# Kernel tuning notes

Hardware: AMD Instinct MI355X
Metric: run time of the kernel (lower is better)

Reference implementation:

```python
import jax, jax.numpy as jnp
import numpy as np

B, H, SQ, SKV, D = 2, 16, 2048, 3072, 64
NUM_PT = 1024  # SKV = NUM_PT + SQ


def setup_inputs() -> dict:
    key = jax.random.key(0)
    kq, kk, kv = jax.random.split(key, 3)
    q = jax.random.normal(kq, (B, H, SQ, D), dtype=jnp.float32)
    k = jax.random.normal(kk, (B, H, SKV, D), dtype=jnp.float32)
    v = jax.random.normal(kv, (B, H, SKV, D), dtype=jnp.float32)
    return {"q": q, "k": k, "v": v, "num_pt": NUM_PT}


def _prefix_causal_mask(sq, skv, num_pt):
    # kv_idx < num_pt always visible (global prefix); otherwise causal on
    # shifted index: q_idx >= kv_idx - num_pt
    q_idx = jnp.arange(sq)[:, None]   # [SQ,1]
    kv_idx = jnp.arange(skv)[None, :]  # [1,SKV]
    return (kv_idx < num_pt) | (q_idx >= kv_idx - num_pt)  # [SQ,SKV]


def reference(q, k, v, num_pt):
    scale = 1.0 / jnp.sqrt(jnp.asarray(q.shape[-1], q.dtype))
    # [B,H,SQ,SKV]
    scores = jnp.einsum("bhqd,bhkd->bhqk", q, k) * scale
    mask = _prefix_causal_mask(q.shape[2], k.shape[2], num_pt)  # [SQ,SKV]
    neg = jnp.asarray(jnp.finfo(scores.dtype).min, scores.dtype)
    scores = jnp.where(mask[None, None], scores, neg)
    probs = jax.nn.softmax(scores, axis=-1)
    return jnp.einsum("bhqk,bhkd->bhqd", probs, v)
```

## Files before the change

### kernel.cpp

```cpp
#include <hip/hip_runtime.h>

#define B_ 2
#define H_ 16
#define SQ_ 2048
#define SKV_ 3072
#define DH 64
#define QT 128
#define KVT 64
#define LDK 72

typedef __attribute__((ext_vector_type(4))) float f32x4;
typedef __attribute__((ext_vector_type(8))) short bf16x8;

__device__ __forceinline__ unsigned cvt_pk(float a, float b) {
  unsigned r;
  asm("v_cvt_pk_bf16_f32 %0, %1, %2" : "=v"(r) : "v"(a), "v"(b));
  return r;
}
__device__ __forceinline__ void pl16_swap(unsigned& a, unsigned& b) {
  asm("v_permlane16_swap_b32 %0, %1" : "+v"(a), "+v"(b));
}
__device__ __forceinline__ void pl32_swap(unsigned& a, unsigned& b) {
  asm("v_permlane32_swap_b32 %0, %1" : "+v"(a), "+v"(b));
}

#define TILE_BODY(T, RK, RV, NK, NV)                                      \
  {                                                                       \
    const int kb  = (T)*KVT;                                              \
    const int buf = (T)&1;                                                \
          \
    {                                                                     \
      int pidx = (T) + 2;                                                 \
      if (pidx > n_tiles - 1) pidx = n_tiles - 1;                         \
      const size_t nb = (size_t)pidx * KVT * DH;                          \
      NK[0] = *(const float4*)(kQp + nb);                                 \
      NK[1] = *(const float4*)(kQp + nb + 4);                             \
      NK[2] = *(const float4*)(kQp + nb + 8);                             \
      NK[3] = *(const float4*)(kQp + nb + 12);                            \
      NV[0] = *(const float4*)(vQp + nb);                                 \
      NV[1] = *(const float4*)(vQp + nb + 4);                             \
      NV[2] = *(const float4*)(vQp + nb + DH);                            \
      NV[3] = *(const float4*)(vQp + nb + DH + 4);                        \
    }                                                                     \
                   \
    f32x4 s0[4], s1[4];                                                   \
    _Pragma("unroll") for (int mg = 0; mg < 4; ++mg) {                    \
      bf16x8 ka0 = *(const bf16x8*)&Ks[buf][mg * 16 + lq][quad * 8];      \
      bf16x8 ka1 = *(const bf16x8*)&Ks[buf][mg * 16 + lq][32 + quad * 8]; \
      f32x4 c0 = (f32x4){0.f, 0.f, 0.f, 0.f};                             \
      f32x4 c1 = (f32x4){0.f, 0.f, 0.f, 0.f};                             \
      c0 = __builtin_amdgcn_mfma_f32_16x16x32_bf16(ka0, qf0[0], c0, 0, 0, 0);\
      c0 = __builtin_amdgcn_mfma_f32_16x16x32_bf16(ka1, qf0[1], c0, 0, 0, 0);\
      c1 = __builtin_amdgcn_mfma_f32_16x16x32_bf16(ka0, qf1[0], c1, 0, 0, 0);\
      c1 = __builtin_amdgcn_mfma_f32_16x16x32_bf16(ka1, qf1[1], c1, 0, 0, 0);\
      s0[mg] = c0; s1[mg] = c1;                                           \
    }                                                                     \
     \
    {                                                                     \
      union { unsigned u[4]; bf16x8 hh; } ta, tb;                         \
      ta.u[0] = cvt_pk(RK[0].x, RK[0].y);                                 \
      ta.u[1] = cvt_pk(RK[0].z, RK[0].w);                                 \
      ta.u[2] = cvt_pk(RK[1].x, RK[1].y);                                 \
      ta.u[3] = cvt_pk(RK[1].z, RK[1].w);                                 \
      *(bf16x8*)&Ks[buf ^ 1][krow][kc] = ta.hh;                           \
      tb.u[0] = cvt_pk(RK[2].x, RK[2].y);                                 \
      tb.u[1] = cvt_pk(RK[2].z, RK[2].w);                                 \
      tb.u[2] = cvt_pk(RK[3].x, RK[3].y);                                 \
      tb.u[3] = cvt_pk(RK[3].z, RK[3].w);                                 \
      *(bf16x8*)&Ks[buf ^ 1][krow][kc + 8] = tb.hh;                       \
      *(unsigned*)&Vt[buf ^ 1][vd0 + 0][2 * vp] = cvt_pk(RV[0].x, RV[2].x);\
      *(unsigned*)&Vt[buf ^ 1][vd0 + 1][2 * vp] = cvt_pk(RV[0].y, RV[2].y);\
      *(unsigned*)&Vt[buf ^ 1][vd0 + 2][2 * vp] = cvt_pk(RV[0].z, RV[2].z);\
      *(unsigned*)&Vt[buf ^ 1][vd0 + 3][2 * vp] = cvt_pk(RV[0].w, RV[2].w);\
      *(unsigned*)&Vt[buf ^ 1][vd0 + 4][2 * vp] = cvt_pk(RV[1].x, RV[3].x);\
      *(unsigned*)&Vt[buf ^ 1][vd0 + 5][2 * vp] = cvt_pk(RV[1].y, RV[3].y);\
      *(unsigned*)&Vt[buf ^ 1][vd0 + 6][2 * vp] = cvt_pk(RV[1].z, RV[3].z);\
      *(unsigned*)&Vt[buf ^ 1][vd0 + 7][2 * vp] = cvt_pk(RV[1].w, RV[3].w);\
    }                                                                     \
                   \
    if (kb + KVT - 1 > q0 + w * 32 + num_pt) {                            \
      _Pragma("unroll") for (int mg = 0; mg < 4; ++mg)                    \
        _Pragma("unroll") for (int r = 0; r < 4; ++r)                     \
          if (kb + mg * 16 + quad * 4 + r > lim0) s0[mg][r] = -__builtin_inff();\
    }                                                                     \
    if (kb + KVT - 1 > q0 + w * 32 + 16 + num_pt) {                       \
      _Pragma("unroll") for (int mg = 0; mg < 4; ++mg)                    \
        _Pragma("unroll") for (int r = 0; r < 4; ++r)                     \
          if (kb + mg * 16 + quad * 4 + r > lim1) s1[mg][r] = -__builtin_inff();\
    }                                                                     \
                                   \
    _Pragma("unroll") for (int mg = 0; mg < 4; ++mg)                      \
      _Pragma("unroll") for (int r = 0; r < 4; ++r) {                     \
        float p0 = __builtin_amdgcn_exp2f(s0[mg][r]);                     \
        float p1 = __builtin_amdgcn_exp2f(s1[mg][r]);                     \
        s0[mg][r] = p0; l40[r] += p0;                                     \
        s1[mg][r] = p1; l41[r] += p1;                                     \
      }                                                                   \
                     \
    union { unsigned u[4]; bf16x8 h; } pa00, pa01, pa10, pa11;            \
    {                                                                     \
      unsigned U[4], W[4];                                                \
      _Pragma("unroll") for (int mg = 0; mg < 4; ++mg) {                  \
        U[mg] = cvt_pk(s0[mg][0], s0[mg][1]);                             \
        W[mg] = cvt_pk(s0[mg][2], s0[mg][3]);                             \
      }                                                                   \
      pl32_swap(U[0], U[1]); pl16_swap(U[0], U[1]);                       \
      pl32_swap(W[0], W[1]); pl16_swap(W[0], W[1]);                       \
      pl32_swap(U[2], U[3]); pl16_swap(U[2], U[3]);                       \
      pl32_swap(W[2], W[3]); pl16_swap(W[2], W[3]);                       \
      pa00.u[0] = U[0]; pa00.u[1] = W[0]; pa00.u[2] = U[1]; pa00.u[3] = W[1];\
      pa01.u[0] = U[2]; pa01.u[1] = W[2]; pa01.u[2] = U[3]; pa01.u[3] = W[3];\
    }                                                                     \
    {                                                                     \
      unsigned U[4], W[4];                                                \
      _Pragma("unroll") for (int mg = 0; mg < 4; ++mg) {                  \
        U[mg] = cvt_pk(s1[mg][0], s1[mg][1]);                             \
        W[mg] = cvt_pk(s1[mg][2], s1[mg][3]);                             \
      }                                                                   \
      pl32_swap(U[0], U[1]); pl16_swap(U[0], U[1]);                       \
      pl32_swap(W[0], W[1]); pl16_swap(W[0], W[1]);                       \
      pl32_swap(U[2], U[3]); pl16_swap(U[2], U[3]);                       \
      pl32_swap(W[2], W[3]); pl16_swap(W[2], W[3]);                       \
      pa10.u[0] = U[0]; pa10.u[1] = W[0]; pa10.u[2] = U[1]; pa10.u[3] = W[1];\
      pa11.u[0] = U[2]; pa11.u[1] = W[2]; pa11.u[2] = U[3]; pa11.u[3] = W[3];\
    }                                                                     \
          \
    _Pragma("unroll") for (int dg = 0; dg < 4; ++dg) {                    \
      bf16x8 vb0 = *(const bf16x8*)&Vt[buf][dg * 16 + lq][quad * 8];      \
      bf16x8 vb1 = *(const bf16x8*)&Vt[buf][dg * 16 + lq][32 + quad * 8]; \
      O0[dg] = __builtin_amdgcn_mfma_f32_16x16x32_bf16(vb0, pa00.h, O0[dg], 0, 0, 0);\
      O0[dg] = __builtin_amdgcn_mfma_f32_16x16x32_bf16(vb1, pa01.h, O0[dg], 0, 0, 0);\
      O1[dg] = __builtin_amdgcn_mfma_f32_16x16x32_bf16(vb0, pa10.h, O1[dg], 0, 0, 0);\
      O1[dg] = __builtin_amdgcn_mfma_f32_16x16x32_bf16(vb1, pa11.h, O1[dg], 0, 0, 0);\
    }                                                                     \
    __syncthreads();                         \
  }

__global__ __launch_bounds__(256, 2) void attn_fwd(
    const float* __restrict__ qg_, const float* __restrict__ kg_,
    const float* __restrict__ vg_, const int* __restrict__ num_pt_p,
    float* __restrict__ og_) {
  __shared__ __align__(16) short Ks[2][KVT][LDK];
  __shared__ __align__(16) short Vt[2][DH][LDK];

  const int tid  = (int)threadIdx.x;
  const int lane = tid & 63;
  const int w    = tid >> 6;
  const int lq   = lane & 15;
  const int quad = lane >> 4;
  const int x    = (int)blockIdx.x;
  const int y    = (int)blockIdx.y;
  const int qb   = (y & 16) ? x : (15 - x);
  const int num_pt = *num_pt_p;
  const int q0   = qb * QT;

  const float* qg = qg_ + (size_t)y * SQ_ * DH;
  const float* kg = kg_ + (size_t)y * SKV_ * DH;
  const float* vg = vg_ + (size_t)y * SKV_ * DH;
  float*       og = og_ + (size_t)y * SQ_ * DH;

  const float SC = 0.125f * 1.44269504088896341f;

  const int qrow0 = q0 + w * 32 + lq;
  const int qrow1 = qrow0 + 16;
  bf16x8 qf0[2], qf1[2];
#pragma unroll
  for (int f = 0; f < 2; ++f) {
    const float* qp = qg + (size_t)(f ? qrow1 : qrow0) * DH + quad * 8;
#pragma unroll
    for (int kh = 0; kh < 2; ++kh) {
      float4 a = *(const float4*)(qp + kh * 32);
      float4 b = *(const float4*)(qp + kh * 32 + 4);
      union { unsigned u[4]; bf16x8 hh; } tq;
      tq.u[0] = cvt_pk(a.x * SC, a.y * SC);
      tq.u[1] = cvt_pk(a.z * SC, a.w * SC);
      tq.u[2] = cvt_pk(b.x * SC, b.y * SC);
      tq.u[3] = cvt_pk(b.z * SC, b.w * SC);
      if (f) qf1[kh] = tq.hh; else qf0[kh] = tq.hh;
    }
  }

  f32x4 O0[4], O1[4];
#pragma unroll
  for (int i = 0; i < 4; ++i) {
    O0[i] = (f32x4){0.f, 0.f, 0.f, 0.f};
    O1[i] = (f32x4){0.f, 0.f, 0.f, 0.f};
  }
  f32x4 l40 = (f32x4){0.f, 0.f, 0.f, 0.f};
  f32x4 l41 = (f32x4){0.f, 0.f, 0.f, 0.f};

  int n_tiles = (q0 + QT - 1 + num_pt) / KVT + 1;
  if (n_tiles > SKV_ / KVT) n_tiles = SKV_ / KVT;

  const int krow = tid >> 2;
  const int kc   = (tid & 3) * 16;
  const int vp   = tid & 31;
  const int vd0  = (tid >> 5) * 8;
  const float* kQp = kg + (size_t)krow * DH + kc;
  const float* vQp = vg + (size_t)(2 * vp) * DH + vd0;

  const int lim0 = qrow0 + num_pt;
  const int lim1 = qrow1 + num_pt;

  float4 Ak[4], Av[4], Bk[4], Bv[4];
  Ak[0] = *(const float4*)(kQp);
  Ak[1] = *(const float4*)(kQp + 4);
  Ak[2] = *(const float4*)(kQp + 8);
  Ak[3] = *(const float4*)(kQp + 12);
  Av[0] = *(const float4*)(vQp);
  Av[1] = *(const float4*)(vQp + 4);
  Av[2] = *(const float4*)(vQp + DH);
  Av[3] = *(const float4*)(vQp + DH + 4);
  {
    const size_t nb = (size_t)KVT * DH;
    Bk[0] = *(const float4*)(kQp + nb);
    Bk[1] = *(const float4*)(kQp + nb + 4);
    Bk[2] = *(const float4*)(kQp + nb + 8);
    Bk[3] = *(const float4*)(kQp + nb + 12);
    Bv[0] = *(const float4*)(vQp + nb);
    Bv[1] = *(const float4*)(vQp + nb + 4);
    Bv[2] = *(const float4*)(vQp + nb + DH);
    Bv[3] = *(const float4*)(vQp + nb + DH + 4);
  }
  {
    union { unsigned u[4]; bf16x8 hh; } ta, tb;
    ta.u[0] = cvt_pk(Ak[0].x, Ak[0].y);
    ta.u[1] = cvt_pk(Ak[0].z, Ak[0].w);
    ta.u[2] = cvt_pk(Ak[1].x, Ak[1].y);
    ta.u[3] = cvt_pk(Ak[1].z, Ak[1].w);
    *(bf16x8*)&Ks[0][krow][kc] = ta.hh;
    tb.u[0] = cvt_pk(Ak[2].x, Ak[2].y);
    tb.u[1] = cvt_pk(Ak[2].z, Ak[2].w);
    tb.u[2] = cvt_pk(Ak[3].x, Ak[3].y);
    tb.u[3] = cvt_pk(Ak[3].z, Ak[3].w);
    *(bf16x8*)&Ks[0][krow][kc + 8] = tb.hh;
    *(unsigned*)&Vt[0][vd0 + 0][2 * vp] = cvt_pk(Av[0].x, Av[2].x);
    *(unsigned*)&Vt[0][vd0 + 1][2 * vp] = cvt_pk(Av[0].y, Av[2].y);
    *(unsigned*)&Vt[0][vd0 + 2][2 * vp] = cvt_pk(Av[0].z, Av[2].z);
    *(unsigned*)&Vt[0][vd0 + 3][2 * vp] = cvt_pk(Av[0].w, Av[2].w);
    *(unsigned*)&Vt[0][vd0 + 4][2 * vp] = cvt_pk(Av[1].x, Av[3].x);
    *(unsigned*)&Vt[0][vd0 + 5][2 * vp] = cvt_pk(Av[1].y, Av[3].y);
    *(unsigned*)&Vt[0][vd0 + 6][2 * vp] = cvt_pk(Av[1].z, Av[3].z);
    *(unsigned*)&Vt[0][vd0 + 7][2 * vp] = cvt_pk(Av[1].w, Av[3].w);
  }
  __syncthreads();

  int t = 0;
  for (; t + 1 < n_tiles; t += 2) {
    TILE_BODY(t,     Bk, Bv, Ak, Av)
    TILE_BODY(t + 1, Ak, Av, Bk, Bv)
  }
  if (t < n_tiles) {
    TILE_BODY(t, Bk, Bv, Ak, Av)
  }

  {
    float lr = l40[0] + l40[1] + l40[2] + l40[3];
    lr += __shfl_xor(lr, 16);
    lr += __shfl_xor(lr, 32);
    float inv = 1.0f / lr;
    float* op = og + (size_t)qrow0 * DH + quad * 4;
#pragma unroll
    for (int dg = 0; dg < 4; ++dg) {
      float4 o4;
      o4.x = O0[dg][0] * inv;
      o4.y = O0[dg][1] * inv;
      o4.z = O0[dg][2] * inv;
      o4.w = O0[dg][3] * inv;
      *(float4*)(op + dg * 16) = o4;
    }
  }
  {
    float lr = l41[0] + l41[1] + l41[2] + l41[3];
    lr += __shfl_xor(lr, 16);
    lr += __shfl_xor(lr, 32);
    float inv = 1.0f / lr;
    float* op = og + (size_t)qrow1 * DH + quad * 4;
#pragma unroll
    for (int dg = 0; dg < 4; ++dg) {
      float4 o4;
      o4.x = O1[dg][0] * inv;
      o4.y = O1[dg][1] * inv;
      o4.z = O1[dg][2] * inv;
      o4.w = O1[dg][3] * inv;
      *(float4*)(op + dg * 16) = o4;
    }
  }
}

extern "C" void kernel_launch(void* const* d_in, const int* in_sizes, int n_in,
                              void* d_out, int out_size, void* d_ws, size_t ws_size,
                              hipStream_t stream) {
  const float* q = (const float*)d_in[0];
  const float* k = (const float*)d_in[1];
  const float* v = (const float*)d_in[2];
  const int* np  = (const int*)d_in[3];
  float* out = (float*)d_out;
  dim3 grid(SQ_ / QT, B_ * H_);
  attn_fwd<<<grid, dim3(256), 0, stream>>>(q, k, v, np, out);
}
```

Baseline: 156.7 us.

## Software-pipeline QK softmax of next tile with PV of current tile

Restructures the KV loop into a three-buffer LDS ring so each iteration computes QK^T and softmax for tile t+1 while doing the PV MFMAs for tile t, staging tile t+2 and prefetching tile t+3 from global. The aim is to overlap exp/convert/permlane work with matrix instructions and reduce dependency stalls. In exchange it uses more LDS (three buffers) and holds two sets of P fragments in registers, which adds register pressure and could lower occupancy at 2 blocks per CU.

Result: slower. 160.2 us (+2.2%).

```diff
diff --git a/kernel.cpp b/kernel.cpp
--- a/kernel.cpp
+++ b/kernel.cpp
@@ -12,6 +12,8 @@
 typedef __attribute__((ext_vector_type(4))) float f32x4;
 typedef __attribute__((ext_vector_type(8))) short bf16x8;
 
+struct PAset { bf16x8 p00, p01, p10, p11; };
+
 __device__ __forceinline__ unsigned cvt_pk(float a, float b) {
   unsigned r;
   asm("v_cvt_pk_bf16_f32 %0, %1, %2" : "=v"(r) : "v"(a), "v"(b));
@@ -24,29 +26,14 @@
   asm("v_permlane32_swap_b32 %0, %1" : "+v"(a), "+v"(b));
 }
 
-#define TILE_BODY(T, RK, RV, NK, NV)                                      \
-  {                                                                       \
-    const int kb  = (T)*KVT;                                              \
-    const int buf = (T)&1;                                                \
-          \
-    {                                                                     \
-      int pidx = (T) + 2;                                                 \
-      if (pidx > n_tiles - 1) pidx = n_tiles - 1;                         \
-      const size_t nb = (size_t)pidx * KVT * DH;                          \
-      NK[0] = *(const float4*)(kQp + nb);                                 \
-      NK[1] = *(const float4*)(kQp + nb + 4);                             \
-      NK[2] = *(const float4*)(kQp + nb + 8);                             \
-      NK[3] = *(const float4*)(kQp + nb + 12);                            \
-      NV[0] = *(const float4*)(vQp + nb);                                 \
-      NV[1] = *(const float4*)(vQp + nb + 4);                             \
-      NV[2] = *(const float4*)(vQp + nb + DH);                            \
-      NV[3] = *(const float4*)(vQp + nb + DH + 4);                        \
-    }                                                                     \
-                   \
+
+#define QKSM(TIDX, KSP, PAS)                                              \
+  {                                                                       \
+    const int kb = (TIDX)*KVT;                                            \
     f32x4 s0[4], s1[4];                                                   \
     _Pragma("unroll") for (int mg = 0; mg < 4; ++mg) {                    \
-      bf16x8 ka0 = *(const bf16x8*)&Ks[buf][mg * 16 + lq][quad * 8];      \
-      bf16x8 ka1 = *(const bf16x8*)&Ks[buf][mg * 16 + lq][32 + quad * 8]; \
+      bf16x8 ka0 = *(const bf16x8*)&KSP[mg * 16 + lq][quad * 8];          \
+      bf16x8 ka1 = *(const bf16x8*)&KSP[mg * 16 + lq][32 + quad * 8];     \
       f32x4 c0 = (f32x4){0.f, 0.f, 0.f, 0.f};                             \
       f32x4 c1 = (f32x4){0.f, 0.f, 0.f, 0.f};                             \
       c0 = __builtin_amdgcn_mfma_f32_16x16x32_bf16(ka0, qf0[0], c0, 0, 0, 0);\
@@ -55,29 +42,6 @@
       c1 = __builtin_amdgcn_mfma_f32_16x16x32_bf16(ka1, qf1[1], c1, 0, 0, 0);\
       s0[mg] = c0; s1[mg] = c1;                                           \
     }                                                                     \
-     \
-    {                                                                     \
-      union { unsigned u[4]; bf16x8 hh; } ta, tb;                         \
-      ta.u[0] = cvt_pk(RK[0].x, RK[0].y);                                 \
-      ta.u[1] = cvt_pk(RK[0].z, RK[0].w);                                 \
-      ta.u[2] = cvt_pk(RK[1].x, RK[1].y);                                 \
-      ta.u[3] = cvt_pk(RK[1].z, RK[1].w);                                 \
-      *(bf16x8*)&Ks[buf ^ 1][krow][kc] = ta.hh;                           \
-      tb.u[0] = cvt_pk(RK[2].x, RK[2].y);                                 \
-      tb.u[1] = cvt_pk(RK[2].z, RK[2].w);                                 \
-      tb.u[2] = cvt_pk(RK[3].x, RK[3].y);                                 \
-      tb.u[3] = cvt_pk(RK[3].z, RK[3].w);                                 \
-      *(bf16x8*)&Ks[buf ^ 1][krow][kc + 8] = tb.hh;                       \
-      *(unsigned*)&Vt[buf ^ 1][vd0 + 0][2 * vp] = cvt_pk(RV[0].x, RV[2].x);\
-      *(unsigned*)&Vt[buf ^ 1][vd0 + 1][2 * vp] = cvt_pk(RV[0].y, RV[2].y);\
-      *(unsigned*)&Vt[buf ^ 1][vd0 + 2][2 * vp] = cvt_pk(RV[0].z, RV[2].z);\
-      *(unsigned*)&Vt[buf ^ 1][vd0 + 3][2 * vp] = cvt_pk(RV[0].w, RV[2].w);\
-      *(unsigned*)&Vt[buf ^ 1][vd0 + 4][2 * vp] = cvt_pk(RV[1].x, RV[3].x);\
-      *(unsigned*)&Vt[buf ^ 1][vd0 + 5][2 * vp] = cvt_pk(RV[1].y, RV[3].y);\
-      *(unsigned*)&Vt[buf ^ 1][vd0 + 6][2 * vp] = cvt_pk(RV[1].z, RV[3].z);\
-      *(unsigned*)&Vt[buf ^ 1][vd0 + 7][2 * vp] = cvt_pk(RV[1].w, RV[3].w);\
-    }                                                                     \
-                   \
     if (kb + KVT - 1 > q0 + w * 32 + num_pt) {                            \
       _Pragma("unroll") for (int mg = 0; mg < 4; ++mg)                    \
         _Pragma("unroll") for (int r = 0; r < 4; ++r)                     \
@@ -88,7 +52,6 @@
         _Pragma("unroll") for (int r = 0; r < 4; ++r)                     \
           if (kb + mg * 16 + quad * 4 + r > lim1) s1[mg][r] = -__builtin_inff();\
     }                                                                     \
-                                   \
     _Pragma("unroll") for (int mg = 0; mg < 4; ++mg)                      \
       _Pragma("unroll") for (int r = 0; r < 4; ++r) {                     \
         float p0 = __builtin_amdgcn_exp2f(s0[mg][r]);                     \
@@ -96,8 +59,6 @@
         s0[mg][r] = p0; l40[r] += p0;                                     \
         s1[mg][r] = p1; l41[r] += p1;                                     \
       }                                                                   \
-                     \
-    union { unsigned u[4]; bf16x8 h; } pa00, pa01, pa10, pa11;            \
     {                                                                     \
       unsigned U[4], W[4];                                                \
       _Pragma("unroll") for (int mg = 0; mg < 4; ++mg) {                  \
@@ -108,8 +69,10 @@
       pl32_swap(W[0], W[1]); pl16_swap(W[0], W[1]);                       \
       pl32_swap(U[2], U[3]); pl16_swap(U[2], U[3]);                       \
       pl32_swap(W[2], W[3]); pl16_swap(W[2], W[3]);                       \
-      pa00.u[0] = U[0]; pa00.u[1] = W[0]; pa00.u[2] = U[1]; pa00.u[3] = W[1];\
-      pa01.u[0] = U[2]; pa01.u[1] = W[2]; pa01.u[2] = U[3]; pa01.u[3] = W[3];\
+      union { unsigned u[4]; bf16x8 h; } t0, t1;                          \
+      t0.u[0] = U[0]; t0.u[1] = W[0]; t0.u[2] = U[1]; t0.u[3] = W[1];     \
+      t1.u[0] = U[2]; t1.u[1] = W[2]; t1.u[2] = U[3]; t1.u[3] = W[3];     \
+      PAS.p00 = t0.h; PAS.p01 = t1.h;                                     \
     }                                                                     \
     {                                                                     \
       unsigned U[4], W[4];                                                \
@@ -121,27 +84,80 @@
       pl32_swap(W[0], W[1]); pl16_swap(W[0], W[1]);                       \
       pl32_swap(U[2], U[3]); pl16_swap(U[2], U[3]);                       \
       pl32_swap(W[2], W[3]); pl16_swap(W[2], W[3]);                       \
-      pa10.u[0] = U[0]; pa10.u[1] = W[0]; pa10.u[2] = U[1]; pa10.u[3] = W[1];\
-      pa11.u[0] = U[2]; pa11.u[1] = W[2]; pa11.u[2] = U[3]; pa11.u[3] = W[3];\
-    }                                                                     \
-          \
+      union { unsigned u[4]; bf16x8 h; } t0, t1;                          \
+      t0.u[0] = U[0]; t0.u[1] = W[0]; t0.u[2] = U[1]; t0.u[3] = W[1];     \
+      t1.u[0] = U[2]; t1.u[1] = W[2]; t1.u[2] = U[3]; t1.u[3] = W[3];     \
+      PAS.p10 = t0.h; PAS.p11 = t1.h;                                     \
+    }                                                                     \
+  }
+
+#define PVACC(VTP, PAS)                                                   \
+  {                                                                       \
     _Pragma("unroll") for (int dg = 0; dg < 4; ++dg) {                    \
-      bf16x8 vb0 = *(const bf16x8*)&Vt[buf][dg * 16 + lq][quad * 8];      \
-      bf16x8 vb1 = *(const bf16x8*)&Vt[buf][dg * 16 + lq][32 + quad * 8]; \
-      O0[dg] = __builtin_amdgcn_mfma_f32_16x16x32_bf16(vb0, pa00.h, O0[dg], 0, 0, 0);\
-      O0[dg] = __builtin_amdgcn_mfma_f32_16x16x32_bf16(vb1, pa01.h, O0[dg], 0, 0, 0);\
-      O1[dg] = __builtin_amdgcn_mfma_f32_16x16x32_bf16(vb0, pa10.h, O1[dg], 0, 0, 0);\
-      O1[dg] = __builtin_amdgcn_mfma_f32_16x16x32_bf16(vb1, pa11.h, O1[dg], 0, 0, 0);\
-    }                                                                     \
-    __syncthreads();                         \
+      bf16x8 vb0 = *(const bf16x8*)&VTP[dg * 16 + lq][quad * 8];          \
+      bf16x8 vb1 = *(const bf16x8*)&VTP[dg * 16 + lq][32 + quad * 8];     \
+      O0[dg] = __builtin_amdgcn_mfma_f32_16x16x32_bf16(vb0, PAS.p00, O0[dg], 0, 0, 0);\
+      O0[dg] = __builtin_amdgcn_mfma_f32_16x16x32_bf16(vb1, PAS.p01, O0[dg], 0, 0, 0);\
+      O1[dg] = __builtin_amdgcn_mfma_f32_16x16x32_bf16(vb0, PAS.p10, O1[dg], 0, 0, 0);\
+      O1[dg] = __builtin_amdgcn_mfma_f32_16x16x32_bf16(vb1, PAS.p11, O1[dg], 0, 0, 0);\
+    }                                                                     \
+  }
+
+#define STAGE(RK, RV, KW, VW)                                             \
+  {                                                                       \
+    union { unsigned u[4]; bf16x8 hh; } ta, tb;                           \
+    ta.u[0] = cvt_pk(RK[0].x, RK[0].y);                                   \
+    ta.u[1] = cvt_pk(RK[0].z, RK[0].w);                                   \
+    ta.u[2] = cvt_pk(RK[1].x, RK[1].y);                                   \
+    ta.u[3] = cvt_pk(RK[1].z, RK[1].w);                                   \
+    *(bf16x8*)&KW[krow][kc] = ta.hh;                                      \
+    tb.u[0] = cvt_pk(RK[2].x, RK[2].y);                                   \
+    tb.u[1] = cvt_pk(RK[2].z, RK[2].w);                                   \
+    tb.u[2] = cvt_pk(RK[3].x, RK[3].y);                                   \
+    tb.u[3] = cvt_pk(RK[3].z, RK[3].w);                                   \
+    *(bf16x8*)&KW[krow][kc + 8] = tb.hh;                                  \
+    *(unsigned*)&VW[vd0 + 0][2 * vp] = cvt_pk(RV[0].x, RV[2].x);          \
+    *(unsigned*)&VW[vd0 + 1][2 * vp] = cvt_pk(RV[0].y, RV[2].y);          \
+    *(unsigned*)&VW[vd0 + 2][2 * vp] = cvt_pk(RV[0].z, RV[2].z);          \
+    *(unsigned*)&VW[vd0 + 3][2 * vp] = cvt_pk(RV[0].w, RV[2].w);          \
+    *(unsigned*)&VW[vd0 + 4][2 * vp] = cvt_pk(RV[1].x, RV[3].x);          \
+    *(unsigned*)&VW[vd0 + 5][2 * vp] = cvt_pk(RV[1].y, RV[3].y);          \
+    *(unsigned*)&VW[vd0 + 6][2 * vp] = cvt_pk(RV[1].z, RV[3].z);          \
+    *(unsigned*)&VW[vd0 + 7][2 * vp] = cvt_pk(RV[1].w, RV[3].w);          \
+  }
+
+#define LOADT(PIDX, NK, NV)                                               \
+  {                                                                       \
+    int pidx = (PIDX);                                                    \
+    if (pidx > n_tiles - 1) pidx = n_tiles - 1;                           \
+    const size_t nb = (size_t)pidx * KVT * DH;                            \
+    NK[0] = *(const float4*)(kQp + nb);                                   \
+    NK[1] = *(const float4*)(kQp + nb + 4);                               \
+    NK[2] = *(const float4*)(kQp + nb + 8);                               \
+    NK[3] = *(const float4*)(kQp + nb + 12);                              \
+    NV[0] = *(const float4*)(vQp + nb);                                   \
+    NV[1] = *(const float4*)(vQp + nb + 4);                               \
+    NV[2] = *(const float4*)(vQp + nb + DH);                              \
+    NV[3] = *(const float4*)(vQp + nb + DH + 4);                          \
+  }
+
+#define BODY(T, RK, RV, NK, NV, PACUR, PANXT)                             \
+  {                                                                       \
+    LOADT((T) + 3, NK, NV)                                                \
+    STAGE(RK, RV, ksC, vtC)                                               \
+    QKSM((T) + 1, ksB, PANXT)                                             \
+    PVACC(vtA, PACUR)                                                     \
+    __syncthreads();                                                      \
+    { short (*tk)[LDK] = ksA; ksA = ksB; ksB = ksC; ksC = tk;             \
+      short (*tv)[LDK] = vtA; vtA = vtB; vtB = vtC; vtC = tv; }           \
   }
 
 __global__ __launch_bounds__(256, 2) void attn_fwd(
     const float* __restrict__ qg_, const float* __restrict__ kg_,
     const float* __restrict__ vg_, const int* __restrict__ num_pt_p,
     float* __restrict__ og_) {
-  __shared__ __align__(16) short Ks[2][KVT][LDK];
-  __shared__ __align__(16) short Vt[2][DH][LDK];
+  __shared__ __align__(16) short KsAll[3][KVT][LDK];
+  __shared__ __align__(16) short VtAll[3][DH][LDK];
 
   const int tid  = (int)threadIdx.x;
   const int lane = tid & 63;
@@ -202,56 +218,31 @@
   const int lim0 = qrow0 + num_pt;
   const int lim1 = qrow1 + num_pt;
 
+  short (*ksA)[LDK] = KsAll[0], (*ksB)[LDK] = KsAll[1], (*ksC)[LDK] = KsAll[2];
+  short (*vtA)[LDK] = VtAll[0], (*vtB)[LDK] = VtAll[1], (*vtC)[LDK] = VtAll[2];
+
   float4 Ak[4], Av[4], Bk[4], Bv[4];
-  Ak[0] = *(const float4*)(kQp);
-  Ak[1] = *(const float4*)(kQp + 4);
-  Ak[2] = *(const float4*)(kQp + 8);
-  Ak[3] = *(const float4*)(kQp + 12);
-  Av[0] = *(const float4*)(vQp);
-  Av[1] = *(const float4*)(vQp + 4);
-  Av[2] = *(const float4*)(vQp + DH);
-  Av[3] = *(const float4*)(vQp + DH + 4);
-  {
-    const size_t nb = (size_t)KVT * DH;
-    Bk[0] = *(const float4*)(kQp + nb);
-    Bk[1] = *(const float4*)(kQp + nb + 4);
-    Bk[2] = *(const float4*)(kQp + nb + 8);
-    Bk[3] = *(const float4*)(kQp + nb + 12);
-    Bv[0] = *(const float4*)(vQp + nb);
-    Bv[1] = *(const float4*)(vQp + nb + 4);
-    Bv[2] = *(const float4*)(vQp + nb + DH);
-    Bv[3] = *(const float4*)(vQp + nb + DH + 4);
-  }
-  {
-    union { unsigned u[4]; bf16x8 hh; } ta, tb;
-    ta.u[0] = cvt_pk(Ak[0].x, Ak[0].y);
-    ta.u[1] = cvt_pk(Ak[0].z, Ak[0].w);
-    ta.u[2] = cvt_pk(Ak[1].x, Ak[1].y);
-    ta.u[3] = cvt_pk(Ak[1].z, Ak[1].w);
-    *(bf16x8*)&Ks[0][krow][kc] = ta.hh;
-    tb.u[0] = cvt_pk(Ak[2].x, Ak[2].y);
-    tb.u[1] = cvt_pk(Ak[2].z, Ak[2].w);
-    tb.u[2] = cvt_pk(Ak[3].x, Ak[3].y);
-    tb.u[3] = cvt_pk(Ak[3].z, Ak[3].w);
-    *(bf16x8*)&Ks[0][krow][kc + 8] = tb.hh;
-    *(unsigned*)&Vt[0][vd0 + 0][2 * vp] = cvt_pk(Av[0].x, Av[2].x);
-    *(unsigned*)&Vt[0][vd0 + 1][2 * vp] = cvt_pk(Av[0].y, Av[2].y);
-    *(unsigned*)&Vt[0][vd0 + 2][2 * vp] = cvt_pk(Av[0].z, Av[2].z);
-    *(unsigned*)&Vt[0][vd0 + 3][2 * vp] = cvt_pk(Av[0].w, Av[2].w);
-    *(unsigned*)&Vt[0][vd0 + 4][2 * vp] = cvt_pk(Av[1].x, Av[3].x);
-    *(unsigned*)&Vt[0][vd0 + 5][2 * vp] = cvt_pk(Av[1].y, Av[3].y);
-    *(unsigned*)&Vt[0][vd0 + 6][2 * vp] = cvt_pk(Av[1].z, Av[3].z);
-    *(unsigned*)&Vt[0][vd0 + 7][2 * vp] = cvt_pk(Av[1].w, Av[3].w);
-  }
+  LOADT(0, Ak, Av)
+  LOADT(1, Bk, Bv)
+  STAGE(Ak, Av, ksA, vtA)
+  STAGE(Bk, Bv, ksB, vtB)
+  LOADT(2, Bk, Bv)
   __syncthreads();
 
+  PAset paE, paO;
+  QKSM(0, ksA, paE)
+
+  const int NB = n_tiles - 1;
   int t = 0;
-  for (; t + 1 < n_tiles; t += 2) {
-    TILE_BODY(t,     Bk, Bv, Ak, Av)
-    TILE_BODY(t + 1, Ak, Av, Bk, Bv)
-  }
-  if (t < n_tiles) {
-    TILE_BODY(t, Bk, Bv, Ak, Av)
+  for (; t + 1 < NB; t += 2) {
+    BODY(t,     Bk, Bv, Ak, Av, paE, paO)
+    BODY(t + 1, Ak, Av, Bk, Bv, paO, paE)
+  }
+  if (t < NB) {
+    BODY(t, Bk, Bv, Ak, Av, paE, paO)
+    PVACC(vtA, paO)
+  } else {
+    PVACC(vtA, paE)
   }
 
   {
```

## Restructure attention tile pipeline with MFMA row-sums, priority hints and peeled tail

Applied to the files above, without the earlier changes.

Splits the per-tile macro into QK, prefetch-load, LDS-stage and softmax/PV stages. The global prefetch of tile t+2 is now issued after the QK MFMAs, and the last tiles are peeled so no clamped redundant loads are issued. Softmax row sums are computed by extra MFMAs against a ones operand instead of VALU adds plus cross-lane shuffles. s_setprio raises wave priority around the MFMA blocks. The aim is to cut VALU work and improve overlap of loads with matrix math, at the cost of four extra MFMAs per tile and more code size.

New measurement: 152.2 us. 2.9% less time.

```diff
diff --git a/kernel.cpp b/kernel.cpp
--- a/kernel.cpp
+++ b/kernel.cpp
@@ -24,26 +24,24 @@
   asm("v_permlane32_swap_b32 %0, %1" : "+v"(a), "+v"(b));
 }
 
-#define TILE_BODY(T, RK, RV, NK, NV)                                      \
-  {                                                                       \
+
+#define SUB_LOAD(NK, NV)                                                  \
+    NK[0] = *(const float4*)(kPf);                                        \
+    NK[1] = *(const float4*)(kPf + 4);                                    \
+    NK[2] = *(const float4*)(kPf + 8);                                    \
+    NK[3] = *(const float4*)(kPf + 12);                                   \
+    NV[0] = *(const float4*)(vPf);                                        \
+    NV[1] = *(const float4*)(vPf + 4);                                    \
+    NV[2] = *(const float4*)(vPf + DH);                                   \
+    NV[3] = *(const float4*)(vPf + DH + 4);                               \
+    kPf += (size_t)KVT * DH;                                              \
+    vPf += (size_t)KVT * DH;
+
+#define SUB_QK(T)                                                         \
     const int kb  = (T)*KVT;                                              \
     const int buf = (T)&1;                                                \
-          \
-    {                                                                     \
-      int pidx = (T) + 2;                                                 \
-      if (pidx > n_tiles - 1) pidx = n_tiles - 1;                         \
-      const size_t nb = (size_t)pidx * KVT * DH;                          \
-      NK[0] = *(const float4*)(kQp + nb);                                 \
-      NK[1] = *(const float4*)(kQp + nb + 4);                             \
-      NK[2] = *(const float4*)(kQp + nb + 8);                             \
-      NK[3] = *(const float4*)(kQp + nb + 12);                            \
-      NV[0] = *(const float4*)(vQp + nb);                                 \
-      NV[1] = *(const float4*)(vQp + nb + 4);                             \
-      NV[2] = *(const float4*)(vQp + nb + DH);                            \
-      NV[3] = *(const float4*)(vQp + nb + DH + 4);                        \
-    }                                                                     \
-                   \
     f32x4 s0[4], s1[4];                                                   \
+    __builtin_amdgcn_s_setprio(1);                                        \
     _Pragma("unroll") for (int mg = 0; mg < 4; ++mg) {                    \
       bf16x8 ka0 = *(const bf16x8*)&Ks[buf][mg * 16 + lq][quad * 8];      \
       bf16x8 ka1 = *(const bf16x8*)&Ks[buf][mg * 16 + lq][32 + quad * 8]; \
@@ -55,7 +53,9 @@
       c1 = __builtin_amdgcn_mfma_f32_16x16x32_bf16(ka1, qf1[1], c1, 0, 0, 0);\
       s0[mg] = c0; s1[mg] = c1;                                           \
     }                                                                     \
-     \
+    __builtin_amdgcn_s_setprio(0);
+
+#define SUB_STAGE(RK, RV)                                                 \
     {                                                                     \
       union { unsigned u[4]; bf16x8 hh; } ta, tb;                         \
       ta.u[0] = cvt_pk(RK[0].x, RK[0].y);                                 \
@@ -76,8 +76,9 @@
       *(unsigned*)&Vt[buf ^ 1][vd0 + 5][2 * vp] = cvt_pk(RV[1].y, RV[3].y);\
       *(unsigned*)&Vt[buf ^ 1][vd0 + 6][2 * vp] = cvt_pk(RV[1].z, RV[3].z);\
       *(unsigned*)&Vt[buf ^ 1][vd0 + 7][2 * vp] = cvt_pk(RV[1].w, RV[3].w);\
-    }                                                                     \
-                   \
+    }
+
+#define SUB_TAIL(T)                                                       \
     if (kb + KVT - 1 > q0 + w * 32 + num_pt) {                            \
       _Pragma("unroll") for (int mg = 0; mg < 4; ++mg)                    \
         _Pragma("unroll") for (int r = 0; r < 4; ++r)                     \
@@ -88,15 +89,11 @@
         _Pragma("unroll") for (int r = 0; r < 4; ++r)                     \
           if (kb + mg * 16 + quad * 4 + r > lim1) s1[mg][r] = -__builtin_inff();\
     }                                                                     \
-                                   \
     _Pragma("unroll") for (int mg = 0; mg < 4; ++mg)                      \
       _Pragma("unroll") for (int r = 0; r < 4; ++r) {                     \
-        float p0 = __builtin_amdgcn_exp2f(s0[mg][r]);                     \
-        float p1 = __builtin_amdgcn_exp2f(s1[mg][r]);                     \
-        s0[mg][r] = p0; l40[r] += p0;                                     \
-        s1[mg][r] = p1; l41[r] += p1;                                     \
+        s0[mg][r] = __builtin_amdgcn_exp2f(s0[mg][r]);                    \
+        s1[mg][r] = __builtin_amdgcn_exp2f(s1[mg][r]);                    \
       }                                                                   \
-                     \
     union { unsigned u[4]; bf16x8 h; } pa00, pa01, pa10, pa11;            \
     {                                                                     \
       unsigned U[4], W[4];                                                \
@@ -124,7 +121,7 @@
       pa10.u[0] = U[0]; pa10.u[1] = W[0]; pa10.u[2] = U[1]; pa10.u[3] = W[1];\
       pa11.u[0] = U[2]; pa11.u[1] = W[2]; pa11.u[2] = U[3]; pa11.u[3] = W[3];\
     }                                                                     \
-          \
+    __builtin_amdgcn_s_setprio(1);                                        \
     _Pragma("unroll") for (int dg = 0; dg < 4; ++dg) {                    \
       bf16x8 vb0 = *(const bf16x8*)&Vt[buf][dg * 16 + lq][quad * 8];      \
       bf16x8 vb1 = *(const bf16x8*)&Vt[buf][dg * 16 + lq][32 + quad * 8]; \
@@ -133,7 +130,30 @@
       O1[dg] = __builtin_amdgcn_mfma_f32_16x16x32_bf16(vb0, pa10.h, O1[dg], 0, 0, 0);\
       O1[dg] = __builtin_amdgcn_mfma_f32_16x16x32_bf16(vb1, pa11.h, O1[dg], 0, 0, 0);\
     }                                                                     \
-    __syncthreads();                         \
+    La = __builtin_amdgcn_mfma_f32_16x16x32_bf16(onesf, pa00.h, La, 0, 0, 0);\
+    La = __builtin_amdgcn_mfma_f32_16x16x32_bf16(onesf, pa01.h, La, 0, 0, 0);\
+    Lb = __builtin_amdgcn_mfma_f32_16x16x32_bf16(onesf, pa10.h, Lb, 0, 0, 0);\
+    Lb = __builtin_amdgcn_mfma_f32_16x16x32_bf16(onesf, pa11.h, Lb, 0, 0, 0);\
+    __builtin_amdgcn_s_setprio(0);                                        \
+    __syncthreads();
+
+#define TILE_PF(T, RK, RV, NK, NV)                                        \
+  {                                                                       \
+    SUB_QK(T)                                                             \
+    SUB_LOAD(NK, NV)                                                      \
+    SUB_STAGE(RK, RV)                                                     \
+    SUB_TAIL(T)                                                           \
+  }
+#define TILE_ST(T, RK, RV)                                                \
+  {                                                                       \
+    SUB_QK(T)                                                             \
+    SUB_STAGE(RK, RV)                                                     \
+    SUB_TAIL(T)                                                           \
+  }
+#define TILE_END(T)                                                       \
+  {                                                                       \
+    SUB_QK(T)                                                             \
+    SUB_TAIL(T)                                                           \
   }
 
 __global__ __launch_bounds__(256, 2) void attn_fwd(
@@ -180,14 +200,17 @@
     }
   }
 
+  const short ob = (short)0x3F80;
+  const bf16x8 onesf = {ob, ob, ob, ob, ob, ob, ob, ob};
+
   f32x4 O0[4], O1[4];
 #pragma unroll
   for (int i = 0; i < 4; ++i) {
     O0[i] = (f32x4){0.f, 0.f, 0.f, 0.f};
     O1[i] = (f32x4){0.f, 0.f, 0.f, 0.f};
   }
-  f32x4 l40 = (f32x4){0.f, 0.f, 0.f, 0.f};
-  f32x4 l41 = (f32x4){0.f, 0.f, 0.f, 0.f};
+  f32x4 La = (f32x4){0.f, 0.f, 0.f, 0.f};
+  f32x4 Lb = (f32x4){0.f, 0.f, 0.f, 0.f};
 
   int n_tiles = (q0 + QT - 1 + num_pt) / KVT + 1;
   if (n_tiles > SKV_ / KVT) n_tiles = SKV_ / KVT;
@@ -223,42 +246,30 @@
     Bv[3] = *(const float4*)(vQp + nb + DH + 4);
   }
   {
-    union { unsigned u[4]; bf16x8 hh; } ta, tb;
-    ta.u[0] = cvt_pk(Ak[0].x, Ak[0].y);
-    ta.u[1] = cvt_pk(Ak[0].z, Ak[0].w);
-    ta.u[2] = cvt_pk(Ak[1].x, Ak[1].y);
-    ta.u[3] = cvt_pk(Ak[1].z, Ak[1].w);
-    *(bf16x8*)&Ks[0][krow][kc] = ta.hh;
-    tb.u[0] = cvt_pk(Ak[2].x, Ak[2].y);
-    tb.u[1] = cvt_pk(Ak[2].z, Ak[2].w);
-    tb.u[2] = cvt_pk(Ak[3].x, Ak[3].y);
-    tb.u[3] = cvt_pk(Ak[3].z, Ak[3].w);
-    *(bf16x8*)&Ks[0][krow][kc + 8] = tb.hh;
-    *(unsigned*)&Vt[0][vd0 + 0][2 * vp] = cvt_pk(Av[0].x, Av[2].x);
-    *(unsigned*)&Vt[0][vd0 + 1][2 * vp] = cvt_pk(Av[0].y, Av[2].y);
-    *(unsigned*)&Vt[0][vd0 + 2][2 * vp] = cvt_pk(Av[0].z, Av[2].z);
-    *(unsigned*)&Vt[0][vd0 + 3][2 * vp] = cvt_pk(Av[0].w, Av[2].w);
-    *(unsigned*)&Vt[0][vd0 + 4][2 * vp] = cvt_pk(Av[1].x, Av[3].x);
-    *(unsigned*)&Vt[0][vd0 + 5][2 * vp] = cvt_pk(Av[1].y, Av[3].y);
-    *(unsigned*)&Vt[0][vd0 + 6][2 * vp] = cvt_pk(Av[1].z, Av[3].z);
-    *(unsigned*)&Vt[0][vd0 + 7][2 * vp] = cvt_pk(Av[1].w, Av[3].w);
+    const int buf = 1;
+    SUB_STAGE(Ak, Av)
   }
   __syncthreads();
 
+  const float* kPf = kQp + (size_t)2 * KVT * DH;
+  const float* vPf = vQp + (size_t)2 * KVT * DH;
+
   int t = 0;
-  for (; t + 1 < n_tiles; t += 2) {
-    TILE_BODY(t,     Bk, Bv, Ak, Av)
-    TILE_BODY(t + 1, Ak, Av, Bk, Bv)
-  }
-  if (t < n_tiles) {
-    TILE_BODY(t, Bk, Bv, Ak, Av)
+  for (; t + 3 < n_tiles; t += 2) {
+    TILE_PF(t,     Bk, Bv, Ak, Av)
+    TILE_PF(t + 1, Ak, Av, Bk, Bv)
+  }
+  if (n_tiles - t == 3) {
+    TILE_PF(t, Bk, Bv, Ak, Av)
+    TILE_ST(t + 1, Ak, Av)
+    TILE_END(t + 2)
+  } else {
+    TILE_ST(t, Bk, Bv)
+    TILE_END(t + 1)
   }
 
   {
-    float lr = l40[0] + l40[1] + l40[2] + l40[3];
-    lr += __shfl_xor(lr, 16);
-    lr += __shfl_xor(lr, 32);
-    float inv = 1.0f / lr;
+    float inv = 1.0f / La[0];
     float* op = og + (size_t)qrow0 * DH + quad * 4;
 #pragma unroll
     for (int dg = 0; dg < 4; ++dg) {
@@ -271,10 +282,7 @@
     }
   }
   {
-    float lr = l41[0] + l41[1] + l41[2] + l41[3];
-    lr += __shfl_xor(lr, 16);
-    lr += __shfl_xor(lr, 32);
-    float inv = 1.0f / lr;
+    float inv = 1.0f / Lb[0];
     float* op = og + (size_t)qrow1 * DH + quad * 4;
 #pragma unroll
     for (int dg = 0; dg < 4; ++dg) {
```
